# Kernel optimization log

Hardware: AMD Instinct MI355X
Metric: run time of the kernel (lower is better)

Reference implementation:

```python
import jax, jax.numpy as jnp
import numpy as np

L, B = 256, 512
K, IN, STATE, OBS = 128, 64, 128, 128


def _preprocess(x, w1, b1, w2, b2):
    # PreProcess: two Linear+ReLU layers mapping raw dim -> k
    t = jax.nn.relu(x @ w1.T + b1)
    return jax.nn.relu(t @ w2.T + b2)


def _dblock_relu(x, w1, b1, w2, b2, wmu, bmu, wls, bls):
    # DBlock (TD-VAE style) with ReLU in place of tanh:
    # t = relu(fc1(x)) * sigmoid(fc2(x)); mu = fc_mu(t); logsigma = fc_logsigma(t)
    t = jax.nn.relu(x @ w1.T + b1) * jax.nn.sigmoid(x @ w2.T + b2)
    return t @ wmu.T + bmu, t @ wls.T + bls


def setup_inputs() -> dict:
    key = jax.random.key(0)
    ks = jax.random.split(key, 24)
    rn = lambda i, shape, s=1.0: jax.random.normal(ks[i], shape, dtype=jnp.float32) * s
    W = 0.05  # small weight scale for numerical stability
    return {
        "external_input_seq": rn(0, (L, B, IN)),
        "observations_seq": rn(1, (L, B, OBS)),
        "eps": rn(2, (L, B, STATE)),
        "u_w1": rn(3, (K, IN), W), "u_b1": jnp.zeros((K,), jnp.float32),
        "u_w2": rn(4, (K, K), W), "u_b2": jnp.zeros((K,), jnp.float32),
        "x_w1": rn(5, (K, OBS), W), "x_b1": jnp.zeros((K,), jnp.float32),
        "x_w2": rn(6, (K, K), W), "x_b2": jnp.zeros((K,), jnp.float32),
        "post_w1": rn(7, (2 * K, 2 * K), W), "post_b1": jnp.zeros((2 * K,), jnp.float32),
        "post_w2": rn(8, (2 * K, 2 * K), W), "post_b2": jnp.zeros((2 * K,), jnp.float32),
        "post_wmu": rn(9, (STATE, 2 * K), W), "post_bmu": jnp.zeros((STATE,), jnp.float32),
        "post_wls": rn(10, (STATE, 2 * K), W), "post_bls": jnp.zeros((STATE,), jnp.float32),
        "gru_wih": rn(11, (3 * K, K), W), "gru_whh": rn(12, (3 * K, K), W),
        "gru_bih": jnp.zeros((3 * K,), jnp.float32), "gru_bhh": jnp.zeros((3 * K,), jnp.float32),
    }


def reference(external_input_seq, observations_seq, eps,
              u_w1, u_b1, u_w2, u_b2,
              x_w1, x_b1, x_w2, x_b2,
              post_w1, post_b1, post_w2, post_b2,
              post_wmu, post_bmu, post_wls, post_bls,
              gru_wih, gru_whh, gru_bih, gru_bhh):
    # _forward_posterior of VAERNN (num_layers=1 GRU)
    u_embed = _preprocess(external_input_seq, u_w1, u_b1, u_w2, u_b2)  # (L,B,K)
    x_embed = _preprocess(observations_seq, x_w1, x_b1, x_w2, x_b2)    # (L,B,K)

    # Precompute input-side GRU gates for all timesteps (one big GEMM)
    x_gates = u_embed @ gru_wih.T + gru_bih  # (L,B,3K)

    h0 = jnp.zeros((external_input_seq.shape[1], K), dtype=external_input_seq.dtype)

    def step(h, xg):
        hg = h @ gru_whh.T + gru_bhh
        xr, xz, xn = jnp.split(xg, 3, axis=-1)
        hr, hz, hn_ = jnp.split(hg, 3, axis=-1)
        r = jax.nn.sigmoid(xr + hr)
        z = jax.nn.sigmoid(xz + hz)
        n = jnp.tanh(xn + r * hn_)
        h_new = (1.0 - z) * n + z * h
        return h_new, h  # emit PRE-update hidden (matches h_seq[:-1])

    hn_final, h_seq = jax.lax.scan(step, h0, x_gates)  # h_seq: (L,B,K)

    # Posterior q(z_t | o_t, h_{t-1}) -- fully parallel over time since z_t
    # never feeds back into the recurrence in this model.
    post_in = jnp.concatenate([x_embed, h_seq], axis=-1)  # (L,B,2K)
    state_mu, state_logsigma = _dblock_relu(
        post_in, post_w1, post_b1, post_w2, post_b2,
        post_wmu, post_bmu, post_wls, post_bls)
    # reparameterized sample from N(mu, diag(exp(logsigma)^2))
    sampled_state = state_mu + jnp.exp(state_logsigma) * eps

    return state_mu, state_logsigma, sampled_state, h_seq, x_embed
```

## Files before the change

### kernel.cpp

```cpp
#include <hip/hip_runtime.h>


typedef __attribute__((ext_vector_type(8))) short bf16x8;
typedef __attribute__((ext_vector_type(4))) short bf16x4;
typedef __attribute__((ext_vector_type(4))) float f32x4;

#define LB 131072

__device__ __forceinline__ short f2b(float f) {
  union { float f; unsigned u; } v; v.f = f;
  unsigned r = (v.u + 0x7FFFu + ((v.u >> 16) & 1u)) >> 16;
  return (short)r;
}
__device__ __forceinline__ float u2f(unsigned u) {
  union { unsigned u; float f; } v; v.u = u << 16; return v.f;
}
__device__ __forceinline__ float rcpf(float x) { return __builtin_amdgcn_rcpf(x); }
__device__ __forceinline__ float exp2f_(float x) { return __builtin_amdgcn_exp2f(x); }
__device__ __forceinline__ float sigm(float x) { return rcpf(1.f + exp2f_(-1.44269504f * x)); }

#define LGKM_BAR()                                          \
  asm volatile("s_waitcnt lgkmcnt(0)" ::: "memory");        \
  __builtin_amdgcn_s_barrier();                             \
  __builtin_amdgcn_sched_barrier(0);

__global__ __launch_bounds__(256) void k_cvt(
    const float* __restrict__ s0, const float* __restrict__ s1,
    const float* __restrict__ s2, const float* __restrict__ s3,
    const float* __restrict__ s4, const float* __restrict__ s5,
    const float* __restrict__ s6, const float* __restrict__ s7,
    const float* __restrict__ s8, const float* __restrict__ s9,
    short* __restrict__ dst)
{
  int i = blockIdx.x * 256 + threadIdx.x;
  if (i >= 352256) return;
  const float* src; int off;
  if      (i <   8192) { src = s0; off = i; }
  else if (i <  24576) { src = s1; off = i - 8192; }
  else if (i <  40960) { src = s2; off = i - 24576; }
  else if (i <  57344) { src = s3; off = i - 40960; }
  else if (i < 106496) { src = s4; off = i - 57344; }
  else if (i < 155648) { src = s5; off = i - 106496; }
  else if (i < 221184) { src = s6; off = i - 155648; }
  else if (i < 286720) { src = s7; off = i - 221184; }
  else if (i < 319488) { src = s8; off = i - 286720; }
  else                 { src = s9; off = i - 319488; }
  dst[i] = f2b(src[off]);
}

#define UT 8
__global__ __launch_bounds__(512) void k_upath(
    const float* __restrict__ x, const short* __restrict__ w1, const float* __restrict__ b1,
    const short* __restrict__ w2, const float* __restrict__ b2,
    const short* __restrict__ wih, const float* __restrict__ bih,
    const float* __restrict__ bhh,
    short* __restrict__ gates)
{
  __shared__ short Xb[32][72];
  __shared__ short Tb[32][136];
  __shared__ short Gb[32][392];
  const int tid = threadIdx.x, w = tid >> 6, l = tid & 63;
  const int lr = l & 15, lg = l >> 4;
  const int n1 = w * 16 + lr;

  bf16x8 wf1[2], wf2[4], wfg[3][4];
  #pragma unroll
  for (int kt = 0; kt < 2; ++kt)
    wf1[kt] = *reinterpret_cast<const bf16x8*>(w1 + (size_t)n1 * 64 + kt * 32 + lg * 8);
  #pragma unroll
  for (int kt = 0; kt < 4; ++kt)
    wf2[kt] = *reinterpret_cast<const bf16x8*>(w2 + (size_t)n1 * 128 + kt * 32 + lg * 8);
  float bgv[3];
  #pragma unroll
  for (int j = 0; j < 3; ++j) {
    const int cg = w * 48 + j * 16 + lr;
    bgv[j] = bih[cg] + (cg < 256 ? bhh[cg] : 0.f);
    #pragma unroll
    for (int kt = 0; kt < 4; ++kt)
      wfg[j][kt] = *reinterpret_cast<const bf16x8*>(wih + (size_t)cg * 128 + kt * 32 + lg * 8);
  }
  const float b1v = b1[n1], b2v = b2[n1];
  const int srow = tid >> 4, scol4 = (tid & 15) * 4, gcol = (tid & 15) * 24;

  for (int it = 0; it < UT; ++it) {
    const size_t m0 = ((size_t)blockIdx.x * UT + it) * 32;

    {
      float4 v = *reinterpret_cast<const float4*>(x + (m0 + srow) * 64 + scol4);
      bf16x4 p; p[0] = f2b(v.x); p[1] = f2b(v.y); p[2] = f2b(v.z); p[3] = f2b(v.w);
      *reinterpret_cast<bf16x4*>(&Xb[srow][scol4]) = p;
    }
    LGKM_BAR();

    f32x4 a1c[2] = {(f32x4){0.f,0.f,0.f,0.f}, (f32x4){0.f,0.f,0.f,0.f}};
    #pragma unroll
    for (int kt = 0; kt < 2; ++kt) {
      #pragma unroll
      for (int mt = 0; mt < 2; ++mt) {
        bf16x8 af = *reinterpret_cast<const bf16x8*>(&Xb[mt * 16 + lr][kt * 32 + lg * 8]);
        a1c[mt] = __builtin_amdgcn_mfma_f32_16x16x32_bf16(af, wf1[kt], a1c[mt], 0, 0, 0);
      }
    }
    #pragma unroll
    for (int mt = 0; mt < 2; ++mt)
      #pragma unroll
      for (int r = 0; r < 4; ++r) {
        float v = a1c[mt][r] + b1v;
        Tb[mt * 16 + lg * 4 + r][n1] = f2b(v > 0.f ? v : 0.f);
      }
    LGKM_BAR();

    f32x4 a2c[2] = {(f32x4){0.f,0.f,0.f,0.f}, (f32x4){0.f,0.f,0.f,0.f}};
    #pragma unroll
    for (int kt = 0; kt < 4; ++kt) {
      #pragma unroll
      for (int mt = 0; mt < 2; ++mt) {
        bf16x8 af = *reinterpret_cast<const bf16x8*>(&Tb[mt * 16 + lr][kt * 32 + lg * 8]);
        a2c[mt] = __builtin_amdgcn_mfma_f32_16x16x32_bf16(af, wf2[kt], a2c[mt], 0, 0, 0);
      }
    }
    #pragma unroll
    for (int mt = 0; mt < 2; ++mt)
      #pragma unroll
      for (int r = 0; r < 4; ++r) {
        float v = a2c[mt][r] + b2v;
        Gb[mt * 16 + lg * 4 + r][n1] = f2b(v > 0.f ? v : 0.f);
      }
    LGKM_BAR();

    bf16x8 ag[2][4];
    #pragma unroll
    for (int mt = 0; mt < 2; ++mt)
      #pragma unroll
      for (int kt = 0; kt < 4; ++kt)
        ag[mt][kt] = *reinterpret_cast<const bf16x8*>(&Gb[mt * 16 + lr][kt * 32 + lg * 8]);
    LGKM_BAR();

    #pragma unroll
    for (int j = 0; j < 3; ++j) {
      #pragma unroll
      for (int mt = 0; mt < 2; ++mt) {
        f32x4 c = {0.f, 0.f, 0.f, 0.f};
        #pragma unroll
        for (int kt = 0; kt < 4; ++kt)
          c = __builtin_amdgcn_mfma_f32_16x16x32_bf16(ag[mt][kt], wfg[j][kt], c, 0, 0, 0);
        #pragma unroll
        for (int r = 0; r < 4; ++r)
          Gb[mt * 16 + lg * 4 + r][w * 48 + j * 16 + lr] = f2b(c[r] + bgv[j]);
      }
    }
    LGKM_BAR();

    #pragma unroll
    for (int k = 0; k < 3; ++k) {
      bf16x8 vv = *reinterpret_cast<const bf16x8*>(&Gb[srow][gcol + k * 8]);
      *reinterpret_cast<bf16x8*>(gates + (m0 + srow) * 384 + gcol + k * 8) = vv;
    }
  }
}

__global__ __launch_bounds__(512) void k_grux(
    const short* __restrict__ gates, const short* __restrict__ whh,
    const float* __restrict__ bhh, float* __restrict__ hseq,
    const float* __restrict__ obs, const short* __restrict__ xw1,
    const float* __restrict__ xb1, const short* __restrict__ xw2,
    const float* __restrict__ xb2, float* __restrict__ xe)
{
  __shared__ short smem_[8 * 32 * 136];
  const int tid = threadIdx.x, w = tid >> 6, l = tid & 63;
  const int lr = l & 15, lg = l >> 4;

  if (blockIdx.x < 128) {
    short (*hb)[16][136] = reinterpret_cast<short (*)[16][136]>(smem_);
    const int m0 = blockIdx.x * 4;
    const int c = w * 16 + lr;
    const int row = lg;
    const size_t gr = m0 + row;

    bf16x8 bfr[3][4];
    #pragma unroll
    for (int g = 0; g < 3; ++g)
      #pragma unroll
      for (int kt = 0; kt < 4; ++kt)
        bfr[g][kt] = *reinterpret_cast<const bf16x8*>(whh + (size_t)(g * 128 + c) * 128 + kt * 32 + lg * 8);
    const float bbn = bhh[256 + c];

    for (int i = tid; i < 2 * 16 * 136; i += 512) smem_[i] = 0;

    float hold = 0.f;

    unsigned gA[3], gB[3];
    #pragma unroll
    for (int g = 0; g < 3; ++g) {
      gA[g] = (unsigned short)gates[gr * 384 + g * 128 + c];
      gB[g] = (unsigned short)gates[(512 + gr) * 384 + g * 128 + c];
    }

    __syncthreads();

#define GRU_STEP(T, GC, BR, BW)                                                \
  {                                                                            \
    const int t_ = (T);                                                        \
    bf16x8 a_[4];                                                              \
    _Pragma("unroll")                                                          \
    for (int kt = 0; kt < 4; ++kt)                                             \
      a_[kt] = *reinterpret_cast<const bf16x8*>(&hb[BR][lr][kt * 32 + lg * 8]);\
    float e_[3];                                                               \
    _Pragma("unroll")                                                          \
    for (int g = 0; g < 3; ++g) {                                              \
      f32x4 cc = {0.f, 0.f, 0.f, 0.f};                                         \
      _Pragma("unroll")                                                        \
      for (int kt = 0; kt < 4; ++kt)                                           \
        cc = __builtin_amdgcn_mfma_f32_16x16x32_bf16(a_[kt], bfr[g][kt], cc, 0, 0, 0); \
    unsigned u0 = __float_as_uint(cc[0]), u2 = __float_as_uint(cc[2]);         \
    unsigned u1 = __float_as_uint(cc[1]), u3 = __float_as_uint(cc[3]);         \
    asm volatile("v_permlane32_swap_b32 %0, %1" : "+v"(u0), "+v"(u2));         \
    asm volatile("v_permlane32_swap_b32 %0, %1" : "+v"(u1), "+v"(u3));         \
    asm volatile("v_permlane16_swap_b32 %0, %1" : "+v"(u0), "+v"(u1));         \
      e_[g] = __uint_as_float(u0);                                             \
    }                                                                          \
    float rr = sigm(u2f(GC[0]) + e_[0]);                                       \
    float zz = sigm(u2f(GC[1]) + e_[1]);                                       \
    float tt = u2f(GC[2]) + (e_[2] + bbn) * rr;                                \
    float nn = 1.f - 2.f * rcpf(1.f + exp2f_(2.88539008f * tt));               \
    float hnew = nn + zz * (hold - nn);                                        \
    hseq[((size_t)t_ * 512 + gr) * 128 + c] = hold;                            \
    hold = hnew;                                                               \
    hb[BW][row][c] = f2b(hnew);                                                \
    const int tp_ = (t_ + 2) & 255;                                            \
    _Pragma("unroll")                                                          \
    for (int g = 0; g < 3; ++g)                                                \
      GC[g] = (unsigned short)gates[((size_t)tp_ * 512 + gr) * 384 + g * 128 + c]; \
    asm volatile("s_waitcnt lgkmcnt(0)" ::: "memory");                         \
    __builtin_amdgcn_s_barrier();                                              \
    __builtin_amdgcn_sched_barrier(0);                                         \
  }

    for (int tt = 0; tt < 128; ++tt) {
      GRU_STEP(2 * tt,     gA, 0, 1)
      GRU_STEP(2 * tt + 1, gB, 1, 0)
    }
#undef GRU_STEP
  } else {
    const int m0 = (blockIdx.x - 128) * 256 + w * 32;
    short (* __restrict__ B)[136] = reinterpret_cast<short (*)[136]>(&smem_[w * 32 * 136]);

    #pragma unroll
    for (int it = 0; it < 16; ++it) {
      int idx = (it * 64 + l) * 4;
      int row = idx >> 7, col = idx & 127;
      float4 v = *reinterpret_cast<const float4*>(obs + (size_t)(m0 + row) * 128 + col);
      bf16x4 p; p[0] = f2b(v.x); p[1] = f2b(v.y); p[2] = f2b(v.z); p[3] = f2b(v.w);
      *reinterpret_cast<bf16x4*>(&B[row][col]) = p;
    }

    f32x4 acc[2][8];
    bf16x8 a1f[2][4];
    #pragma unroll
    for (int mt = 0; mt < 2; ++mt)
      #pragma unroll
      for (int kt = 0; kt < 4; ++kt)
        a1f[mt][kt] = *reinterpret_cast<const bf16x8*>(&B[mt * 16 + lr][kt * 32 + lg * 8]);
    #pragma unroll
    for (int nt = 0; nt < 8; ++nt)
      #pragma unroll
      for (int mt = 0; mt < 2; ++mt) {
        f32x4 c = {0.f, 0.f, 0.f, 0.f};
        #pragma unroll
        for (int kt = 0; kt < 4; ++kt) {
          bf16x8 bv = *reinterpret_cast<const bf16x8*>(xw1 + (size_t)(nt * 16 + lr) * 128 + kt * 32 + lg * 8);
          c = __builtin_amdgcn_mfma_f32_16x16x32_bf16(a1f[mt][kt], bv, c, 0, 0, 0);
        }
        acc[mt][nt] = c;
      }
    #pragma unroll
    for (int nt = 0; nt < 8; ++nt) {
      float bb = xb1[nt * 16 + lr];
      #pragma unroll
      for (int mt = 0; mt < 2; ++mt)
        #pragma unroll
        for (int r = 0; r < 4; ++r) {
          float v = acc[mt][nt][r] + bb;
          B[mt * 16 + lg * 4 + r][nt * 16 + lr] = f2b(v > 0.f ? v : 0.f);
        }
    }

    bf16x8 a2f[2][4];
    #pragma unroll
    for (int mt = 0; mt < 2; ++mt)
      #pragma unroll
      for (int kt = 0; kt < 4; ++kt)
        a2f[mt][kt] = *reinterpret_cast<const bf16x8*>(&B[mt * 16 + lr][kt * 32 + lg * 8]);
    #pragma unroll
    for (int nt = 0; nt < 8; ++nt) {
      float bb = xb2[nt * 16 + lr];
      #pragma unroll
      for (int mt = 0; mt < 2; ++mt) {
        f32x4 c = {0.f, 0.f, 0.f, 0.f};
        #pragma unroll
        for (int kt = 0; kt < 4; ++kt) {
          bf16x8 bv = *reinterpret_cast<const bf16x8*>(xw2 + (size_t)(nt * 16 + lr) * 128 + kt * 32 + lg * 8);
          c = __builtin_amdgcn_mfma_f32_16x16x32_bf16(a2f[mt][kt], bv, c, 0, 0, 0);
        }
        #pragma unroll
        for (int r = 0; r < 4; ++r) {
          float v = c[r] + bb;
          xe[(size_t)(m0 + mt * 16 + lg * 4 + r) * 128 + nt * 16 + lr] = (v > 0.f ? v : 0.f);
        }
      }
    }
  }
}

#define PT 8
__global__ __launch_bounds__(512) void k_post(
    const float* __restrict__ xe, const float* __restrict__ hs, const float* __restrict__ eps,
    const short* __restrict__ pw1, const float* __restrict__ pb1,
    const short* __restrict__ pw2, const float* __restrict__ pb2,
    const short* __restrict__ pwmu, const float* __restrict__ pbmu,
    const short* __restrict__ pwls, const float* __restrict__ pbls,
    float* __restrict__ mu, float* __restrict__ ls, float* __restrict__ samp)
{
  __shared__ short Ab[32][264];
  const int tid = threadIdx.x, w = tid >> 6, l = tid & 63;
  const int lr = l & 15, lg = l >> 4;
  const int srow = tid >> 4, scol = (tid & 15) * 8;
  const int n2 = w * 16 + lr;

  bf16x8 wf1[2][8];
  float bb1[2], bb2[2];
  #pragma unroll
  for (int j = 0; j < 2; ++j) {
    const int n = w * 32 + j * 16 + lr;
    bb1[j] = pb1[n]; bb2[j] = pb2[n];
    #pragma unroll
    for (int kt = 0; kt < 8; ++kt)
      wf1[j][kt] = *reinterpret_cast<const bf16x8*>(pw1 + (size_t)n * 256 + kt * 32 + lg * 8);
  }
  const float bbm = pbmu[n2], bbl = pbls[n2];

  for (int it = 0; it < PT; ++it) {
    const size_t m0 = ((size_t)blockIdx.x * PT + it) * 32;

    unsigned long long a2 = (unsigned long long)pw2;
    unsigned long long am_ = (unsigned long long)pwmu;
    unsigned long long al_ = (unsigned long long)pwls;
    asm volatile("" : "+s"(a2), "+s"(am_), "+s"(al_));
    const short* pw2v = (const short*)a2;
    const short* pwmv = (const short*)am_;
    const short* pwlv = (const short*)al_;

    float ev[2][4];
    #pragma unroll
    for (int mt = 0; mt < 2; ++mt)
      #pragma unroll
      for (int r = 0; r < 4; ++r)
        ev[mt][r] = eps[(m0 + mt * 16 + lg * 4 + r) * 128 + n2];

    {
      const float* px = xe + (m0 + srow) * 128 + scol;
      float4 v0 = *reinterpret_cast<const float4*>(px);
      float4 v1 = *reinterpret_cast<const float4*>(px + 4);
      bf16x8 pk;
      pk[0] = f2b(v0.x); pk[1] = f2b(v0.y); pk[2] = f2b(v0.z); pk[3] = f2b(v0.w);
      pk[4] = f2b(v1.x); pk[5] = f2b(v1.y); pk[6] = f2b(v1.z); pk[7] = f2b(v1.w);
      *reinterpret_cast<bf16x8*>(&Ab[srow][scol]) = pk;
      const float* ph = hs + (m0 + srow) * 128 + scol;
      float4 h0 = *reinterpret_cast<const float4*>(ph);
      float4 h1 = *reinterpret_cast<const float4*>(ph + 4);
      bf16x8 qk;
      qk[0] = f2b(h0.x); qk[1] = f2b(h0.y); qk[2] = f2b(h0.z); qk[3] = f2b(h0.w);
      qk[4] = f2b(h1.x); qk[5] = f2b(h1.y); qk[6] = f2b(h1.z); qk[7] = f2b(h1.w);
      *reinterpret_cast<bf16x8*>(&Ab[srow][128 + scol]) = qk;
    }
    LGKM_BAR();

    bf16x8 wf2[2][8];
    #pragma unroll
    for (int j = 0; j < 2; ++j) {
      const int n = w * 32 + j * 16 + lr;
      #pragma unroll
      for (int kt = 0; kt < 8; ++kt)
        wf2[j][kt] = *reinterpret_cast<const bf16x8*>(pw2v + (size_t)n * 256 + kt * 32 + lg * 8);
    }
    f32x4 ac1[2][2], ac2[2][2];
    #pragma unroll
    for (int j = 0; j < 2; ++j)
      #pragma unroll
      for (int mt = 0; mt < 2; ++mt) { ac1[j][mt] = (f32x4){0.f,0.f,0.f,0.f}; ac2[j][mt] = (f32x4){0.f,0.f,0.f,0.f}; }
    #pragma unroll
    for (int kt = 0; kt < 8; ++kt) {
      bf16x8 af[2];
      #pragma unroll
      for (int mt = 0; mt < 2; ++mt)
        af[mt] = *reinterpret_cast<const bf16x8*>(&Ab[mt * 16 + lr][kt * 32 + lg * 8]);
      #pragma unroll
      for (int j = 0; j < 2; ++j)
        #pragma unroll
        for (int mt = 0; mt < 2; ++mt) {
          ac1[j][mt] = __builtin_amdgcn_mfma_f32_16x16x32_bf16(af[mt], wf1[j][kt], ac1[j][mt], 0, 0, 0);
          ac2[j][mt] = __builtin_amdgcn_mfma_f32_16x16x32_bf16(af[mt], wf2[j][kt], ac2[j][mt], 0, 0, 0);
        }
    }

    bf16x8 wm[8], wl[8];
    #pragma unroll
    for (int kt = 0; kt < 8; ++kt) {
      wm[kt] = *reinterpret_cast<const bf16x8*>(pwmv + (size_t)n2 * 256 + kt * 32 + lg * 8);
      wl[kt] = *reinterpret_cast<const bf16x8*>(pwlv + (size_t)n2 * 256 + kt * 32 + lg * 8);
    }
    LGKM_BAR();

    #pragma unroll
    for (int j = 0; j < 2; ++j)
      #pragma unroll
      for (int mt = 0; mt < 2; ++mt)
        #pragma unroll
        for (int r = 0; r < 4; ++r) {
          float t1 = ac1[j][mt][r] + bb1[j]; t1 = t1 > 0.f ? t1 : 0.f;
          float t2 = sigm(ac2[j][mt][r] + bb2[j]);
          Ab[mt * 16 + lg * 4 + r][w * 32 + j * 16 + lr] = f2b(t1 * t2);
        }
    LGKM_BAR();

    f32x4 amc[2], alc[2];
    #pragma unroll
    for (int mt = 0; mt < 2; ++mt) { amc[mt] = (f32x4){0.f,0.f,0.f,0.f}; alc[mt] = (f32x4){0.f,0.f,0.f,0.f}; }
    #pragma unroll
    for (int kt = 0; kt < 8; ++kt) {
      bf16x8 at[2];
      #pragma unroll
      for (int mt = 0; mt < 2; ++mt)
        at[mt] = *reinterpret_cast<const bf16x8*>(&Ab[mt * 16 + lr][kt * 32 + lg * 8]);
      #pragma unroll
      for (int mt = 0; mt < 2; ++mt) {
        amc[mt] = __builtin_amdgcn_mfma_f32_16x16x32_bf16(at[mt], wm[kt], amc[mt], 0, 0, 0);
        alc[mt] = __builtin_amdgcn_mfma_f32_16x16x32_bf16(at[mt], wl[kt], alc[mt], 0, 0, 0);
      }
    }
    #pragma unroll
    for (int mt = 0; mt < 2; ++mt)
      #pragma unroll
      for (int r = 0; r < 4; ++r) {
        size_t off = (m0 + mt * 16 + lg * 4 + r) * 128 + n2;
        float m_ = amc[mt][r] + bbm;
        float l_ = alc[mt][r] + bbl;
        mu[off] = m_;
        ls[off] = l_;
        samp[off] = m_ + exp2f_(1.44269504f * l_) * ev[mt][r];
      }
    LGKM_BAR();
  }
}

extern "C" void kernel_launch(void* const* d_in, const int* in_sizes, int n_in,
                              void* d_out, int out_size, void* d_ws, size_t ws_size,
                              hipStream_t stream) {
  const float* ext   = (const float*)d_in[0];
  const float* obs   = (const float*)d_in[1];
  const float* eps   = (const float*)d_in[2];
  const float* u_w1  = (const float*)d_in[3];
  const float* u_b1  = (const float*)d_in[4];
  const float* u_w2  = (const float*)d_in[5];
  const float* u_b2  = (const float*)d_in[6];
  const float* x_w1  = (const float*)d_in[7];
  const float* x_b1  = (const float*)d_in[8];
  const float* x_w2  = (const float*)d_in[9];
  const float* x_b2  = (const float*)d_in[10];
  const float* pw1   = (const float*)d_in[11];
  const float* pb1   = (const float*)d_in[12];
  const float* pw2   = (const float*)d_in[13];
  const float* pb2   = (const float*)d_in[14];
  const float* pwmu  = (const float*)d_in[15];
  const float* pbmu  = (const float*)d_in[16];
  const float* pwls  = (const float*)d_in[17];
  const float* pbls  = (const float*)d_in[18];
  const float* g_wih = (const float*)d_in[19];
  const float* g_whh = (const float*)d_in[20];
  const float* g_bih = (const float*)d_in[21];
  const float* g_bhh = (const float*)d_in[22];

  float* out = (float*)d_out;
  float* o_mu = out;
  float* o_ls = out + 16777216;
  float* o_sp = out + 33554432;
  float* o_hs = out + 50331648;
  float* o_xe = out + 67108864;
  short* gates = (short*)out;

  short* wb = (short*)d_ws;
  short* c_uw1  = wb + 0;
  short* c_uw2  = wb + 8192;
  short* c_xw1  = wb + 24576;
  short* c_xw2  = wb + 40960;
  short* c_wih  = wb + 57344;
  short* c_whh  = wb + 106496;
  short* c_pw1  = wb + 155648;
  short* c_pw2  = wb + 221184;
  short* c_pwmu = wb + 286720;
  short* c_pwls = wb + 319488;

  k_cvt<<<1376, 256, 0, stream>>>(u_w1, u_w2, x_w1, x_w2, g_wih, g_whh,
                                  pw1, pw2, pwmu, pwls, wb);
  k_upath<<<512, 512, 0, stream>>>(ext, c_uw1, u_b1, c_uw2, u_b2, c_wih, g_bih, g_bhh, gates);
  k_grux<<<640, 512, 0, stream>>>(gates, c_whh, g_bhh, o_hs,
                                  obs, c_xw1, x_b1, c_xw2, x_b2, o_xe);
  k_post<<<512, 512, 0, stream>>>(o_xe, o_hs, eps, c_pw1, pb1, c_pw2, pb2,
                                  c_pwmu, pbmu, c_pwls, pbls, o_mu, o_ls, o_sp);
}
```

Before: 412.4 us.

## Split GRU gate MFMA chains and shrink per-block tiles for more blocks

In the serial GRU recurrence, each gate's four dependent MFMAs become two independent accumulation chains that are summed afterwards. The gates are now computed in the order r, n, z so the sigmoid and tanh math can overlap the remaining matrix work, and the hidden-state write to shared memory moves earlier. Separately, the per-block tile count in the u-path and posterior kernels drops from 8 to 2, with four times as many blocks launched. This raises parallelism, at the cost of reloading weight fragments into registers more often per block.

```diff
diff --git a/kernel.cpp b/kernel.cpp
--- a/kernel.cpp
+++ b/kernel.cpp
@@ -48,7 +48,7 @@
   dst[i] = f2b(src[off]);
 }
 
-#define UT 8
+#define UT 2
 __global__ __launch_bounds__(512) void k_upath(
     const float* __restrict__ x, const short* __restrict__ w1, const float* __restrict__ b1,
     const short* __restrict__ w2, const float* __restrict__ b2,
@@ -198,6 +198,22 @@
 
     __syncthreads();
 
+#define GATE_E(G, OUT)                                                         \
+  {                                                                            \
+    f32x4 cA = {0.f, 0.f, 0.f, 0.f}, cB = {0.f, 0.f, 0.f, 0.f};               \
+    cA = __builtin_amdgcn_mfma_f32_16x16x32_bf16(a_[0], bfr[G][0], cA, 0, 0, 0); \
+    cB = __builtin_amdgcn_mfma_f32_16x16x32_bf16(a_[2], bfr[G][2], cB, 0, 0, 0); \
+    cA = __builtin_amdgcn_mfma_f32_16x16x32_bf16(a_[1], bfr[G][1], cA, 0, 0, 0); \
+    cB = __builtin_amdgcn_mfma_f32_16x16x32_bf16(a_[3], bfr[G][3], cB, 0, 0, 0); \
+    f32x4 cc = cA + cB;                                                        \
+    unsigned u0 = __float_as_uint(cc[0]), u2 = __float_as_uint(cc[2]);         \
+    unsigned u1 = __float_as_uint(cc[1]), u3 = __float_as_uint(cc[3]);         \
+    asm volatile("v_permlane32_swap_b32 %0, %1" : "+v"(u0), "+v"(u2));         \
+    asm volatile("v_permlane32_swap_b32 %0, %1" : "+v"(u1), "+v"(u3));         \
+    asm volatile("v_permlane16_swap_b32 %0, %1" : "+v"(u0), "+v"(u1));         \
+    OUT = __uint_as_float(u0);                                                 \
+  }
+
 #define GRU_STEP(T, GC, BR, BW)                                                \
   {                                                                            \
     const int t_ = (T);                                                        \
@@ -205,28 +221,18 @@
     _Pragma("unroll")                                                          \
     for (int kt = 0; kt < 4; ++kt)                                             \
       a_[kt] = *reinterpret_cast<const bf16x8*>(&hb[BR][lr][kt * 32 + lg * 8]);\
-    float e_[3];                                                               \
-    _Pragma("unroll")                                                          \
-    for (int g = 0; g < 3; ++g) {                                              \
-      f32x4 cc = {0.f, 0.f, 0.f, 0.f};                                         \
-      _Pragma("unroll")                                                        \
-      for (int kt = 0; kt < 4; ++kt)                                           \
-        cc = __builtin_amdgcn_mfma_f32_16x16x32_bf16(a_[kt], bfr[g][kt], cc, 0, 0, 0); \
-    unsigned u0 = __float_as_uint(cc[0]), u2 = __float_as_uint(cc[2]);         \
-    unsigned u1 = __float_as_uint(cc[1]), u3 = __float_as_uint(cc[3]);         \
-    asm volatile("v_permlane32_swap_b32 %0, %1" : "+v"(u0), "+v"(u2));         \
-    asm volatile("v_permlane32_swap_b32 %0, %1" : "+v"(u1), "+v"(u3));         \
-    asm volatile("v_permlane16_swap_b32 %0, %1" : "+v"(u0), "+v"(u1));         \
-      e_[g] = __uint_as_float(u0);                                             \
-    }                                                                          \
-    float rr = sigm(u2f(GC[0]) + e_[0]);                                       \
-    float zz = sigm(u2f(GC[1]) + e_[1]);                                       \
-    float tt = u2f(GC[2]) + (e_[2] + bbn) * rr;                                \
+    float e0, e1, e2;                                                          \
+    GATE_E(0, e0)                            \
+    float rr = sigm(u2f(GC[0]) + e0);                                          \
+    GATE_E(2, e2)                                           \
+    float tt = u2f(GC[2]) + (e2 + bbn) * rr;                                   \
     float nn = 1.f - 2.f * rcpf(1.f + exp2f_(2.88539008f * tt));               \
+    GATE_E(1, e1)                         \
+    float zz = sigm(u2f(GC[1]) + e1);                                          \
     float hnew = nn + zz * (hold - nn);                                        \
+    hb[BW][row][c] = f2b(hnew);           \
     hseq[((size_t)t_ * 512 + gr) * 128 + c] = hold;                            \
     hold = hnew;                                                               \
-    hb[BW][row][c] = f2b(hnew);                                                \
     const int tp_ = (t_ + 2) & 255;                                            \
     _Pragma("unroll")                                                          \
     for (int g = 0; g < 3; ++g)                                                \
@@ -241,6 +247,7 @@
       GRU_STEP(2 * tt + 1, gB, 1, 0)
     }
 #undef GRU_STEP
+#undef GATE_E
   } else {
     const int m0 = (blockIdx.x - 128) * 256 + w * 32;
     short (* __restrict__ B)[136] = reinterpret_cast<short (*)[136]>(&smem_[w * 32 * 136]);
@@ -312,7 +319,7 @@
   }
 }
 
-#define PT 8
+#define PT 2
 __global__ __launch_bounds__(512) void k_post(
     const float* __restrict__ xe, const float* __restrict__ hs, const float* __restrict__ eps,
     const short* __restrict__ pw1, const float* __restrict__ pb1,
@@ -502,9 +509,9 @@
 
   k_cvt<<<1376, 256, 0, stream>>>(u_w1, u_w2, x_w1, x_w2, g_wih, g_whh,
                                   pw1, pw2, pwmu, pwls, wb);
-  k_upath<<<512, 512, 0, stream>>>(ext, c_uw1, u_b1, c_uw2, u_b2, c_wih, g_bih, g_bhh, gates);
+  k_upath<<<2048, 512, 0, stream>>>(ext, c_uw1, u_b1, c_uw2, u_b2, c_wih, g_bih, g_bhh, gates);
   k_grux<<<640, 512, 0, stream>>>(gates, c_whh, g_bhh, o_hs,
                                   obs, c_xw1, x_b1, c_xw2, x_b2, o_xe);
-  k_post<<<512, 512, 0, stream>>>(o_xe, o_hs, eps, c_pw1, pb1, c_pw2, pb2,
-                                  c_pwmu, pbmu, c_pwls, pbls, o_mu, o_ls, o_sp);
-}
+  k_post<<<2048, 512, 0, stream>>>(o_xe, o_hs, eps, c_pw1, pb1, c_pw2, pb2,
+                                   c_pwmu, pbmu, c_pwls, pbls, o_mu, o_ls, o_sp);
+}
```

New measurement: 435.7 us. +5.7%, slower.
